# Kernel optimization log

Hardware: AMD Instinct MI355X
Metric: run time of the kernel (lower is better)

The kernel has to match this reference:

```python
import jax, jax.numpy as jnp
import numpy as np
import math

# ---- static circuit structure ----
N_QUBITS = 12
N_STATES = 1 << N_QUBITS
NUM_HEADS = 4
HEAD_DIM = N_QUBITS // NUM_HEADS
EPS = 1e-5

# convention: wire 0 = most significant bit of the basis index
_idx = np.arange(N_STATES)
_bits = (_idx[:, None] >> (N_QUBITS - 1 - np.arange(N_QUBITS))) & 1  # (N_STATES, n)
SIGNS = jnp.asarray((1 - 2 * _bits).astype(np.float32))  # +1 for |0>, -1 for |1>

# compose the CNOT ring [(0,1),(1,2),...,(n-2,n-1),(n-1,0)] into a single basis permutation.
# each CNOT(c,t) maps basis b -> b xor (bit_c(b) << pos_t); applying gate G: new[b] = old[sigma(b)].
_perm = _idx.copy()
_gates = [(i, i + 1) for i in range(N_QUBITS - 1)] + [(N_QUBITS - 1, 0)]
for _c, _t in reversed(_gates):
    _bc = (_idx >> (N_QUBITS - 1 - _c)) & 1
    _sigma = _idx ^ (_bc << (N_QUBITS - 1 - _t))
    _perm = _sigma[_perm]
PERM = jnp.asarray(_perm.astype(np.int32))
# second rx layer uses params token[wire % head_dim]
FOLD = np.arange(N_QUBITS) % HEAD_DIM


def _ring_z(theta):
    """Per-token circuit: RX(theta_k) on wire k (the two consecutive RX layers are
    pre-summed into theta), then CNOT ring, then <Z_k> for every wire.
    Product-state probabilities suffice: CNOTs only permute the computational basis.
    theta: (..., n_qubits) -> (..., n_qubits) expectation values."""
    shp = theta.shape
    T = theta.reshape(-1, N_QUBITS)
    h = 0.5 * T
    p0 = jnp.cos(h) ** 2  # P(|0>) per qubit after RX(theta)|0>
    p1 = jnp.sin(h) ** 2
    probs = jnp.ones((T.shape[0], 1), T.dtype)
    for k in range(N_QUBITS):  # kron build, wire 0 is MSB -> (tokens, 2^n)
        pk = jnp.stack([p0[:, k], p1[:, k]], axis=-1)
        probs = (probs[:, :, None] * pk[:, None, :]).reshape(T.shape[0], -1)
    probs = probs[:, PERM]  # apply CNOT ring as basis permutation
    return (probs @ SIGNS).reshape(shp)


def _layernorm(x, g, b):
    mu = jnp.mean(x, axis=-1, keepdims=True)
    var = jnp.mean((x - mu) ** 2, axis=-1, keepdims=True)
    return (x - mu) * jax.lax.rsqrt(var + EPS) * g + b


def _forward(x, wq, wk, wv, wo, w1, b1, w2, b2, g1, be1, g2, be2):
    B, S, E = x.shape
    # multi-head attention (dropout in eval mode = identity)
    q = (x @ wq).reshape(B, S, NUM_HEADS, HEAD_DIM).transpose(0, 2, 1, 3)
    k = (x @ wk).reshape(B, S, NUM_HEADS, HEAD_DIM).transpose(0, 2, 1, 3)
    v = (x @ wv).reshape(B, S, NUM_HEADS, HEAD_DIM).transpose(0, 2, 1, 3)
    scores = jnp.einsum('bhqd,bhkd->bhqk', q, k) / math.sqrt(HEAD_DIM)
    attn = jax.nn.softmax(scores, axis=-1)
    o = jnp.einsum('bhqk,bhkd->bhqd', attn, v).transpose(0, 2, 1, 3).reshape(B, S, E)
    # per-token quantum circuit: encoder RX(o_k) then RX(o_{k % head_dim}) combine additively
    theta = o + o[..., FOLD]
    attn_out = _ring_z(theta) @ wo
    x1 = _layernorm(x + attn_out, g1, be1)
    # quantum FFN: RX(h_k) then RY(h_k) on |0>, no entangler -> <Z_k> = cos(h_k)*cos(h_k)
    hdn = jax.nn.relu(x1 @ w1 + b1)
    zq = jnp.cos(hdn) * jnp.cos(hdn)
    ffn_out = zq @ w2 + b2
    return _layernorm(x1 + ffn_out, g2, be2)


def setup_inputs() -> dict:
    key = jax.random.key(0)
    ks = jax.random.split(key, 8)
    E = N_QUBITS
    F = N_QUBITS  # ffn_dim forced equal to n_qubits by the source
    s = 1.0 / math.sqrt(E)
    return {
        'x': jax.random.normal(ks[0], (4, 2048, E), jnp.float32),
        'wq': jax.random.normal(ks[1], (E, E), jnp.float32) * s,
        'wk': jax.random.normal(ks[2], (E, E), jnp.float32) * s,
        'wv': jax.random.normal(ks[3], (E, E), jnp.float32) * s,
        'wo': jax.random.normal(ks[4], (E, E), jnp.float32) * s,
        'w1': jax.random.normal(ks[5], (E, F), jnp.float32) * s,
        'b1': jnp.zeros((F,), jnp.float32),
        'w2': jax.random.normal(ks[6], (F, E), jnp.float32) * (1.0 / math.sqrt(F)),
        'b2': jnp.zeros((E,), jnp.float32),
        'g1': jnp.ones((E,), jnp.float32),
        'be1': jnp.zeros((E,), jnp.float32),
        'g2': jnp.ones((E,), jnp.float32),
        'be2': jnp.zeros((E,), jnp.float32),
    }


def reference(x, wq, wk, wv, wo, w1, b1, w2, b2, g1, be1, g2, be2):
    return _forward(x, wq, wk, wv, wo, w1, b1, w2, b2, g1, be1, g2, be2)
```

## Files before the change

### kernel.cpp

```cpp
#include <hip/hip_runtime.h>
#include <math.h>

#define S_LEN 2048
#define NH 4
#define BHN 16
#define E_DIM 12
#define NKB 8
#define KEYS_PER_KB (S_LEN / NKB)
#define NQT 8
#define QT_SIZE (S_LEN / NQT)
#define QSCALE 0.8329931278350429f

typedef float f32x2 __attribute__((ext_vector_type(2)));

static __device__ __forceinline__ f32x2 pk_mul_blo(f32x2 a, f32x2 b) {
    f32x2 d; asm("v_pk_mul_f32 %0, %1, %2 op_sel_hi:[1,0]"
                 : "=v"(d) : "v"(a), "v"(b)); return d;
}
static __device__ __forceinline__ f32x2 pk_fma_blo(f32x2 a, f32x2 b, f32x2 c) {
    f32x2 d; asm("v_pk_fma_f32 %0, %1, %2, %3 op_sel_hi:[1,0,1]"
                 : "=v"(d) : "v"(a), "v"(b), "v"(c)); return d;
}
static __device__ __forceinline__ f32x2 pk_fma_bhi(f32x2 a, f32x2 b, f32x2 c) {
    f32x2 d; asm("v_pk_fma_f32 %0, %1, %2, %3 op_sel:[0,1,0] op_sel_hi:[1,1,1]"
                 : "=v"(d) : "v"(a), "v"(b), "v"(c)); return d;
}
static __device__ __forceinline__ f32x2 pk_add2(f32x2 a, f32x2 b) {
    f32x2 d; asm("v_pk_add_f32 %0, %1, %2"
                 : "=v"(d) : "v"(a), "v"(b)); return d;
}

__global__ __launch_bounds__(256, 6) void attn_kernel(
    const float* __restrict__ x,
    const float* __restrict__ wq, const float* __restrict__ wk,
    const float* __restrict__ wv, float4* __restrict__ part)
{
    __shared__ __align__(16) char smem[16384];
    float4* sK  = (float4*)smem;
    float4* sV  = sK + KEYS_PER_KB;
    float4* sQ  = sV + KEYS_PER_KB;
    float*  sw  = (float*)(smem + 12288);
    float4* sAcc = (float4*)smem;

    int tid = threadIdx.x;
    int kb = blockIdx.x & (NKB - 1);
    int qt = (blockIdx.x / NKB) & (NQT - 1);
    int bh = blockIdx.x / (NKB * NQT);
    int b  = bh >> 2;
    int h  = bh & 3;

    if (tid < 108) {
        int m = tid / 36;
        int i = tid - m * 36;
        int e = i / 3, d = i - e * 3;
        const float* w = (m == 0) ? wq : (m == 1) ? wk : wv;
        sw[tid] = w[e * 12 + h * 3 + d];
    }
    __syncthreads();

    {
        size_t kt = (size_t)b * S_LEN + kb * KEYS_PER_KB + tid;
        const float4* xp = (const float4*)(x + kt * E_DIM);
        float4 xa = xp[0], xb = xp[1], xc = xp[2];
        float xr[12] = {xa.x, xa.y, xa.z, xa.w, xb.x, xb.y, xb.z, xb.w, xc.x, xc.y, xc.z, xc.w};
        float k0 = 0, k1 = 0, k2 = 0, v0 = 0, v1 = 0, v2 = 0;
#pragma unroll
        for (int e = 0; e < 12; ++e) {
            float xe = xr[e];
            k0 = fmaf(xe, sw[36 + e * 3 + 0], k0);
            k1 = fmaf(xe, sw[36 + e * 3 + 1], k1);
            k2 = fmaf(xe, sw[36 + e * 3 + 2], k2);
            v0 = fmaf(xe, sw[72 + e * 3 + 0], v0);
            v1 = fmaf(xe, sw[72 + e * 3 + 1], v1);
            v2 = fmaf(xe, sw[72 + e * 3 + 2], v2);
        }
        sK[tid] = make_float4(k0, k1, k2, 0.0f);
        sV[tid] = make_float4(v0, v1, v2, 0.0f);

        size_t qtk = (size_t)b * S_LEN + qt * QT_SIZE + tid;
        const float4* xq = (const float4*)(x + qtk * E_DIM);
        float4 qa = xq[0], qb = xq[1], qc = xq[2];
        float qr[12] = {qa.x, qa.y, qa.z, qa.w, qb.x, qb.y, qb.z, qb.w, qc.x, qc.y, qc.z, qc.w};
        float q0 = 0, q1 = 0, q2 = 0;
#pragma unroll
        for (int e = 0; e < 12; ++e) {
            float xe = qr[e];
            q0 = fmaf(xe, sw[e * 3 + 0], q0);
            q1 = fmaf(xe, sw[e * 3 + 1], q1);
            q2 = fmaf(xe, sw[e * 3 + 2], q2);
        }
        sQ[tid] = make_float4(q0 * QSCALE, q1 * QSCALE, q2 * QSCALE, 0.0f);
    }
    __syncthreads();

    int w = tid >> 6;
    int lane = tid & 63;

    float4 q0 = sQ[0 * 64 + lane];
    float4 q1 = sQ[1 * 64 + lane];
    float4 q2 = sQ[2 * 64 + lane];
    float4 q3 = sQ[3 * 64 + lane];
    f32x2 qx01 = {q0.x, q1.x}, qy01 = {q0.y, q1.y}, qz01 = {q0.z, q1.z};
    f32x2 qx23 = {q2.x, q3.x}, qy23 = {q2.y, q3.y}, qz23 = {q2.z, q3.z};

    f32x2 ax01 = {0,0}, ay01 = {0,0}, az01 = {0,0}, ad01 = {0,0};
    f32x2 ax23 = {0,0}, ay23 = {0,0}, az23 = {0,0}, ad23 = {0,0};

    int kbeg = w * 64;
#pragma unroll 4
    for (int j = 0; j < 64; ++j) {
        float4 kk = sK[kbeg + j];
        float4 vv = sV[kbeg + j];
        f32x2 kxy = {kk.x, kk.y};
        f32x2 kzw = {kk.z, kk.w};
        f32x2 vxy = {vv.x, vv.y};
        f32x2 vzw = {vv.z, vv.w};
        f32x2 s01 = pk_mul_blo(qz01, kzw);
        s01 = pk_fma_bhi(qy01, kxy, s01);
        s01 = pk_fma_blo(qx01, kxy, s01);
        f32x2 s23 = pk_mul_blo(qz23, kzw);
        s23 = pk_fma_bhi(qy23, kxy, s23);
        s23 = pk_fma_blo(qx23, kxy, s23);
        f32x2 p01, p23;
        p01.x = __builtin_amdgcn_exp2f(s01.x);
        p01.y = __builtin_amdgcn_exp2f(s01.y);
        p23.x = __builtin_amdgcn_exp2f(s23.x);
        p23.y = __builtin_amdgcn_exp2f(s23.y);
        ax01 = pk_fma_blo(p01, vxy, ax01);
        ay01 = pk_fma_bhi(p01, vxy, ay01);
        az01 = pk_fma_blo(p01, vzw, az01);
        ad01 = pk_add2(p01, ad01);
        ax23 = pk_fma_blo(p23, vxy, ax23);
        ay23 = pk_fma_bhi(p23, vxy, ay23);
        az23 = pk_fma_blo(p23, vzw, az23);
        ad23 = pk_add2(p23, ad23);
    }

    __syncthreads();
    sAcc[w * QT_SIZE + 0 * 64 + lane] = make_float4(ax01.x, ay01.x, az01.x, ad01.x);
    sAcc[w * QT_SIZE + 1 * 64 + lane] = make_float4(ax01.y, ay01.y, az01.y, ad01.y);
    sAcc[w * QT_SIZE + 2 * 64 + lane] = make_float4(ax23.x, ay23.x, az23.x, ad23.x);
    sAcc[w * QT_SIZE + 3 * 64 + lane] = make_float4(ax23.y, ay23.y, az23.y, ad23.y);
    __syncthreads();

    float4 sum = sAcc[tid];
    float4 p1 = sAcc[QT_SIZE + tid];
    float4 p2 = sAcc[2 * QT_SIZE + tid];
    float4 p3 = sAcc[3 * QT_SIZE + tid];
    sum.x += p1.x + p2.x + p3.x;
    sum.y += p1.y + p2.y + p3.y;
    sum.z += p1.z + p2.z + p3.z;
    sum.w += p1.w + p2.w + p3.w;

    part[((size_t)kb * BHN + bh) * S_LEN + qt * QT_SIZE + tid] = sum;
}

__global__ __launch_bounds__(64) void tail_kernel(
    const float4* __restrict__ part, const float* __restrict__ x,
    const float* __restrict__ wo, const float* __restrict__ w1, const float* __restrict__ b1,
    const float* __restrict__ w2, const float* __restrict__ b2,
    const float* __restrict__ g1, const float* __restrict__ be1,
    const float* __restrict__ g2, const float* __restrict__ be2,
    float* __restrict__ out)
{
    __shared__ float swo[144], sw1[144], sw2[144];
    __shared__ float sb1[12], sb2[12], sg1[12], sbe1[12], sg2[12], sbe2[12];
    int tid = threadIdx.x;
    for (int i = tid; i < 144; i += 64) { swo[i] = wo[i]; sw1[i] = w1[i]; sw2[i] = w2[i]; }
    if (tid < 12) {
        sb1[tid] = b1[tid]; sb2[tid] = b2[tid];
        sg1[tid] = g1[tid]; sbe1[tid] = be1[tid];
        sg2[tid] = g2[tid]; sbe2[tid] = be2[tid];
    }
    __syncthreads();

    int t = blockIdx.x * 64 + tid;
    int b = t >> 11;
    int s = t & (S_LEN - 1);

    float o[12];
#pragma unroll
    for (int h = 0; h < NH; ++h) {
        int bh = b * NH + h;
        float ax = 0, ay = 0, az = 0, aw = 0;
#pragma unroll
        for (int kb = 0; kb < NKB; ++kb) {
            float4 p = part[((size_t)kb * BHN + bh) * S_LEN + s];
            ax += p.x; ay += p.y; az += p.z; aw += p.w;
        }
        float inv = 1.0f / aw;
        o[h * 3 + 0] = ax * inv;
        o[h * 3 + 1] = ay * inv;
        o[h * 3 + 2] = az * inv;
    }

    float c[12];
#pragma unroll
    for (int k = 0; k < 12; ++k) c[k] = __cosf(o[k] + o[k % 3]);

    float z[12];
    {
        float p = c[0];
#pragma unroll
        for (int k = 1; k < 12; ++k) { p *= c[k]; z[k] = p; }
        p = c[1];
#pragma unroll
        for (int k = 2; k < 12; ++k) p *= c[k];
        z[0] = p;
    }

    const float4* xp = (const float4*)(x + (size_t)t * E_DIM);
    float4 xa = xp[0], xb = xp[1], xc = xp[2];
    float xr[12] = {xa.x, xa.y, xa.z, xa.w, xb.x, xb.y, xb.z, xb.w, xc.x, xc.y, xc.z, xc.w};

    float y[12];
#pragma unroll
    for (int e = 0; e < 12; ++e) {
        float ao = 0;
#pragma unroll
        for (int k = 0; k < 12; ++k) ao = fmaf(z[k], swo[k * 12 + e], ao);
        y[e] = xr[e] + ao;
    }

    float mu = 0;
#pragma unroll
    for (int e = 0; e < 12; ++e) mu += y[e];
    mu *= (1.0f / 12.0f);
    float var = 0;
#pragma unroll
    for (int e = 0; e < 12; ++e) { float d = y[e] - mu; var = fmaf(d, d, var); }
    var *= (1.0f / 12.0f);
    float rs = rsqrtf(var + 1e-5f);
    float x1v[12];
#pragma unroll
    for (int e = 0; e < 12; ++e) x1v[e] = (y[e] - mu) * rs * sg1[e] + sbe1[e];

    float zq[12];
#pragma unroll
    for (int f = 0; f < 12; ++f) {
        float hd = sb1[f];
#pragma unroll
        for (int e = 0; e < 12; ++e) hd = fmaf(x1v[e], sw1[e * 12 + f], hd);
        hd = fmaxf(hd, 0.0f);
        float cc = __cosf(hd);
        zq[f] = cc * cc;
    }
    float y2[12];
#pragma unroll
    for (int e = 0; e < 12; ++e) {
        float fo = sb2[e];
#pragma unroll
        for (int f = 0; f < 12; ++f) fo = fmaf(zq[f], sw2[f * 12 + e], fo);
        y2[e] = x1v[e] + fo;
    }

    float mu2 = 0;
#pragma unroll
    for (int e = 0; e < 12; ++e) mu2 += y2[e];
    mu2 *= (1.0f / 12.0f);
    float var2 = 0;
#pragma unroll
    for (int e = 0; e < 12; ++e) { float d = y2[e] - mu2; var2 = fmaf(d, d, var2); }
    var2 *= (1.0f / 12.0f);
    float rs2 = rsqrtf(var2 + 1e-5f);

    float res[12];
#pragma unroll
    for (int e = 0; e < 12; ++e) res[e] = (y2[e] - mu2) * rs2 * sg2[e] + sbe2[e];

    float4* op = (float4*)(out + (size_t)t * E_DIM);
    op[0] = make_float4(res[0], res[1], res[2], res[3]);
    op[1] = make_float4(res[4], res[5], res[6], res[7]);
    op[2] = make_float4(res[8], res[9], res[10], res[11]);
}

extern "C" void kernel_launch(void* const* d_in, const int* in_sizes, int n_in,
                              void* d_out, int out_size, void* d_ws, size_t ws_size,
                              hipStream_t stream)
{
    const float* x   = (const float*)d_in[0];
    const float* wq  = (const float*)d_in[1];
    const float* wk  = (const float*)d_in[2];
    const float* wv  = (const float*)d_in[3];
    const float* wo  = (const float*)d_in[4];
    const float* w1  = (const float*)d_in[5];
    const float* b1  = (const float*)d_in[6];
    const float* w2  = (const float*)d_in[7];
    const float* b2  = (const float*)d_in[8];
    const float* g1  = (const float*)d_in[9];
    const float* be1 = (const float*)d_in[10];
    const float* g2  = (const float*)d_in[11];
    const float* be2 = (const float*)d_in[12];

    float4* part = (float4*)d_ws;

    attn_kernel<<<BHN * NQT * NKB, 256, 0, stream>>>(x, wq, wk, wv, part);
    tail_kernel<<<128, 64, 0, stream>>>(part, x, wo, w1, b1, w2, b2,
                                        g1, be1, g2, be2, (float*)d_out);
}
```

Before: 25.91 us.

## Fuse tail into attention kernel via last-block atomic counter, halve query tiles

Merges the separate tail kernel into the attention kernel. Each block writes its partial with non-temporal stores and bumps an atomic counter per (batch, query tile); the 32nd block to finish reduces the partials and runs the output projection, layernorms and FFN. The query tile is doubled to 512 (NQT 4), so each thread handles 8 queries per key and the grid shrinks to 512 blocks. This removes one kernel launch and overlaps the tail with attention, but adds a memset launch, serialises the tail on a few last blocks, and raises register pressure.

```diff
diff --git a/kernel.cpp b/kernel.cpp
--- a/kernel.cpp
+++ b/kernel.cpp
@@ -7,11 +7,12 @@
 #define E_DIM 12
 #define NKB 8
 #define KEYS_PER_KB (S_LEN / NKB)
-#define NQT 8
+#define NQT 4
 #define QT_SIZE (S_LEN / NQT)
 #define QSCALE 0.8329931278350429f
 
 typedef float f32x2 __attribute__((ext_vector_type(2)));
+typedef float f32x4 __attribute__((ext_vector_type(4)));
 
 static __device__ __forceinline__ f32x2 pk_mul_blo(f32x2 a, f32x2 b) {
     f32x2 d; asm("v_pk_mul_f32 %0, %1, %2 op_sel_hi:[1,0]"
@@ -30,17 +31,50 @@
                  : "=v"(d) : "v"(a), "v"(b)); return d;
 }
 
-__global__ __launch_bounds__(256, 6) void attn_kernel(
+static __device__ __forceinline__ void store_nt(f32x4* p, f32x4 v) {
+    asm volatile("global_store_dwordx4 %0, %1, off sc0 sc1 nt"
+                 :: "v"(p), "v"(v) : "memory");
+}
+static __device__ __forceinline__ f32x4 load_sc_issue(const f32x4* p) {
+    f32x4 d;
+    asm volatile("global_load_dwordx4 %0, %1, off sc0 sc1"
+                 : "=v"(d) : "v"(p) : "memory");
+    return d;
+}
+
+#define PAIR_STEP(QX,QY,QZ,AX,AY,AZ,AD) do {                       \
+    f32x2 s_ = pk_mul_blo(QZ, kzw);                                \
+    s_ = pk_fma_bhi(QY, kxy, s_);                                  \
+    s_ = pk_fma_blo(QX, kxy, s_);                                  \
+    f32x2 p_;                                                      \
+    p_.x = __builtin_amdgcn_exp2f(s_.x);                           \
+    p_.y = __builtin_amdgcn_exp2f(s_.y);                           \
+    AX = pk_fma_blo(p_, vxy, AX);                                  \
+    AY = pk_fma_bhi(p_, vxy, AY);                                  \
+    AZ = pk_fma_blo(p_, vzw, AZ);                                  \
+    AD = pk_add2(p_, AD);                                          \
+} while (0)
+
+__global__ __launch_bounds__(256) void attn_fused_kernel(
     const float* __restrict__ x,
     const float* __restrict__ wq, const float* __restrict__ wk,
-    const float* __restrict__ wv, float4* __restrict__ part)
+    const float* __restrict__ wv, const float* __restrict__ wo,
+    const float* __restrict__ w1, const float* __restrict__ b1,
+    const float* __restrict__ w2, const float* __restrict__ b2,
+    const float* __restrict__ g1, const float* __restrict__ be1,
+    const float* __restrict__ g2, const float* __restrict__ be2,
+    f32x4* __restrict__ part, unsigned int* __restrict__ counter,
+    float* __restrict__ out)
 {
-    __shared__ __align__(16) char smem[16384];
-    float4* sK  = (float4*)smem;
-    float4* sV  = sK + KEYS_PER_KB;
-    float4* sQ  = sV + KEYS_PER_KB;
-    float*  sw  = (float*)(smem + 12288);
+    __shared__ __align__(16) char smem[32768];
+    float4* sK = (float4*)smem;
+    float4* sV = sK + KEYS_PER_KB;
+    float4* sQ = sV + KEYS_PER_KB;
+    float*  sw = (float*)(smem + 16384);
     float4* sAcc = (float4*)smem;
+    __shared__ float swo[144], sw1[144], sw2[144];
+    __shared__ float sb1[12], sb2[12], sg1[12], sbe1[12], sg2[12], sbe2[12];
+    __shared__ int sLast;
 
     int tid = threadIdx.x;
     int kb = blockIdx.x & (NKB - 1);
@@ -77,96 +111,94 @@
         sK[tid] = make_float4(k0, k1, k2, 0.0f);
         sV[tid] = make_float4(v0, v1, v2, 0.0f);
 
-        size_t qtk = (size_t)b * S_LEN + qt * QT_SIZE + tid;
-        const float4* xq = (const float4*)(x + qtk * E_DIM);
-        float4 qa = xq[0], qb = xq[1], qc = xq[2];
-        float qr[12] = {qa.x, qa.y, qa.z, qa.w, qb.x, qb.y, qb.z, qb.w, qc.x, qc.y, qc.z, qc.w};
-        float q0 = 0, q1 = 0, q2 = 0;
-#pragma unroll
-        for (int e = 0; e < 12; ++e) {
-            float xe = qr[e];
-            q0 = fmaf(xe, sw[e * 3 + 0], q0);
-            q1 = fmaf(xe, sw[e * 3 + 1], q1);
-            q2 = fmaf(xe, sw[e * 3 + 2], q2);
-        }
-        sQ[tid] = make_float4(q0 * QSCALE, q1 * QSCALE, q2 * QSCALE, 0.0f);
+#pragma unroll
+        for (int rr = 0; rr < 2; ++rr) {
+            int qi = rr * 256 + tid;
+            size_t qtk = (size_t)b * S_LEN + qt * QT_SIZE + qi;
+            const float4* xq = (const float4*)(x + qtk * E_DIM);
+            float4 qa = xq[0], qb = xq[1], qc = xq[2];
+            float qr[12] = {qa.x, qa.y, qa.z, qa.w, qb.x, qb.y, qb.z, qb.w, qc.x, qc.y, qc.z, qc.w};
+            float q0 = 0, q1 = 0, q2 = 0;
+#pragma unroll
+            for (int e = 0; e < 12; ++e) {
+                float xe = qr[e];
+                q0 = fmaf(xe, sw[e * 3 + 0], q0);
+                q1 = fmaf(xe, sw[e * 3 + 1], q1);
+                q2 = fmaf(xe, sw[e * 3 + 2], q2);
+            }
+            sQ[qi] = make_float4(q0 * QSCALE, q1 * QSCALE, q2 * QSCALE, 0.0f);
+        }
     }
     __syncthreads();
 
     int w = tid >> 6;
     int lane = tid & 63;
 
-    float4 q0 = sQ[0 * 64 + lane];
-    float4 q1 = sQ[1 * 64 + lane];
-    float4 q2 = sQ[2 * 64 + lane];
-    float4 q3 = sQ[3 * 64 + lane];
+    float4 q0 = sQ[0 * 64 + lane], q1 = sQ[1 * 64 + lane];
+    float4 q2 = sQ[2 * 64 + lane], q3 = sQ[3 * 64 + lane];
+    float4 q4 = sQ[4 * 64 + lane], q5 = sQ[5 * 64 + lane];
+    float4 q6 = sQ[6 * 64 + lane], q7 = sQ[7 * 64 + lane];
     f32x2 qx01 = {q0.x, q1.x}, qy01 = {q0.y, q1.y}, qz01 = {q0.z, q1.z};
     f32x2 qx23 = {q2.x, q3.x}, qy23 = {q2.y, q3.y}, qz23 = {q2.z, q3.z};
+    f32x2 qx45 = {q4.x, q5.x}, qy45 = {q4.y, q5.y}, qz45 = {q4.z, q5.z};
+    f32x2 qx67 = {q6.x, q7.x}, qy67 = {q6.y, q7.y}, qz67 = {q6.z, q7.z};
 
     f32x2 ax01 = {0,0}, ay01 = {0,0}, az01 = {0,0}, ad01 = {0,0};
     f32x2 ax23 = {0,0}, ay23 = {0,0}, az23 = {0,0}, ad23 = {0,0};
+    f32x2 ax45 = {0,0}, ay45 = {0,0}, az45 = {0,0}, ad45 = {0,0};
+    f32x2 ax67 = {0,0}, ay67 = {0,0}, az67 = {0,0}, ad67 = {0,0};
 
     int kbeg = w * 64;
-#pragma unroll 4
+#pragma unroll 2
     for (int j = 0; j < 64; ++j) {
         float4 kk = sK[kbeg + j];
         float4 vv = sV[kbeg + j];
-        f32x2 kxy = {kk.x, kk.y};
-        f32x2 kzw = {kk.z, kk.w};
-        f32x2 vxy = {vv.x, vv.y};
-        f32x2 vzw = {vv.z, vv.w};
-        f32x2 s01 = pk_mul_blo(qz01, kzw);
-        s01 = pk_fma_bhi(qy01, kxy, s01);
-        s01 = pk_fma_blo(qx01, kxy, s01);
-        f32x2 s23 = pk_mul_blo(qz23, kzw);
-        s23 = pk_fma_bhi(qy23, kxy, s23);
-        s23 = pk_fma_blo(qx23, kxy, s23);
-        f32x2 p01, p23;
-        p01.x = __builtin_amdgcn_exp2f(s01.x);
-        p01.y = __builtin_amdgcn_exp2f(s01.y);
-        p23.x = __builtin_amdgcn_exp2f(s23.x);
-        p23.y = __builtin_amdgcn_exp2f(s23.y);
-        ax01 = pk_fma_blo(p01, vxy, ax01);
-        ay01 = pk_fma_bhi(p01, vxy, ay01);
-        az01 = pk_fma_blo(p01, vzw, az01);
-        ad01 = pk_add2(p01, ad01);
-        ax23 = pk_fma_blo(p23, vxy, ax23);
-        ay23 = pk_fma_bhi(p23, vxy, ay23);
-        az23 = pk_fma_blo(p23, vzw, az23);
-        ad23 = pk_add2(p23, ad23);
-    }
-
-    __syncthreads();
-    sAcc[w * QT_SIZE + 0 * 64 + lane] = make_float4(ax01.x, ay01.x, az01.x, ad01.x);
-    sAcc[w * QT_SIZE + 1 * 64 + lane] = make_float4(ax01.y, ay01.y, az01.y, ad01.y);
-    sAcc[w * QT_SIZE + 2 * 64 + lane] = make_float4(ax23.x, ay23.x, az23.x, ad23.x);
-    sAcc[w * QT_SIZE + 3 * 64 + lane] = make_float4(ax23.y, ay23.y, az23.y, ad23.y);
-    __syncthreads();
-
-    float4 sum = sAcc[tid];
-    float4 p1 = sAcc[QT_SIZE + tid];
-    float4 p2 = sAcc[2 * QT_SIZE + tid];
-    float4 p3 = sAcc[3 * QT_SIZE + tid];
-    sum.x += p1.x + p2.x + p3.x;
-    sum.y += p1.y + p2.y + p3.y;
-    sum.z += p1.z + p2.z + p3.z;
-    sum.w += p1.w + p2.w + p3.w;
-
-    part[((size_t)kb * BHN + bh) * S_LEN + qt * QT_SIZE + tid] = sum;
-}
-
-__global__ __launch_bounds__(64) void tail_kernel(
-    const float4* __restrict__ part, const float* __restrict__ x,
-    const float* __restrict__ wo, const float* __restrict__ w1, const float* __restrict__ b1,
-    const float* __restrict__ w2, const float* __restrict__ b2,
-    const float* __restrict__ g1, const float* __restrict__ be1,
-    const float* __restrict__ g2, const float* __restrict__ be2,
-    float* __restrict__ out)
-{
-    __shared__ float swo[144], sw1[144], sw2[144];
-    __shared__ float sb1[12], sb2[12], sg1[12], sbe1[12], sg2[12], sbe2[12];
-    int tid = threadIdx.x;
-    for (int i = tid; i < 144; i += 64) { swo[i] = wo[i]; sw1[i] = w1[i]; sw2[i] = w2[i]; }
+        f32x2 kxy = {kk.x, kk.y}, kzw = {kk.z, kk.w};
+        f32x2 vxy = {vv.x, vv.y}, vzw = {vv.z, vv.w};
+        PAIR_STEP(qx01, qy01, qz01, ax01, ay01, az01, ad01);
+        PAIR_STEP(qx23, qy23, qz23, ax23, ay23, az23, ad23);
+        PAIR_STEP(qx45, qy45, qz45, ax45, ay45, az45, ad45);
+        PAIR_STEP(qx67, qy67, qz67, ax67, ay67, az67, ad67);
+    }
+
+    __syncthreads();
+    {
+        float4* a = sAcc + w * QT_SIZE + lane;
+        a[0 * 64] = make_float4(ax01.x, ay01.x, az01.x, ad01.x);
+        a[1 * 64] = make_float4(ax01.y, ay01.y, az01.y, ad01.y);
+        a[2 * 64] = make_float4(ax23.x, ay23.x, az23.x, ad23.x);
+        a[3 * 64] = make_float4(ax23.y, ay23.y, az23.y, ad23.y);
+        a[4 * 64] = make_float4(ax45.x, ay45.x, az45.x, ad45.x);
+        a[5 * 64] = make_float4(ax45.y, ay45.y, az45.y, ad45.y);
+        a[6 * 64] = make_float4(ax67.x, ay67.x, az67.x, ad67.x);
+        a[7 * 64] = make_float4(ax67.y, ay67.y, az67.y, ad67.y);
+    }
+    __syncthreads();
+
+#pragma unroll
+    for (int rr = 0; rr < 2; ++rr) {
+        int qq = rr * 256 + tid;
+        float4 sum = sAcc[qq];
+        float4 p1 = sAcc[QT_SIZE + qq];
+        float4 p2 = sAcc[2 * QT_SIZE + qq];
+        float4 p3 = sAcc[3 * QT_SIZE + qq];
+        f32x4 sv;
+        sv.x = sum.x + (p1.x + p2.x + p3.x);
+        sv.y = sum.y + (p1.y + p2.y + p3.y);
+        sv.z = sum.z + (p1.z + p2.z + p3.z);
+        sv.w = sum.w + (p1.w + p2.w + p3.w);
+        store_nt(part + ((size_t)kb * BHN + bh) * S_LEN + qt * QT_SIZE + qq, sv);
+    }
+    __syncthreads();
+
+    if (tid == 0) {
+        unsigned old = atomicAdd(&counter[b * NQT + qt], 1u);
+        sLast = (old == 31u);
+    }
+    __syncthreads();
+    if (!sLast) return;
+
+    for (int i = tid; i < 144; i += 256) { swo[i] = wo[i]; sw1[i] = w1[i]; sw2[i] = w2[i]; }
     if (tid < 12) {
         sb1[tid] = b1[tid]; sb2[tid] = b2[tid];
         sg1[tid] = g1[tid]; sbe1[tid] = be1[tid];
@@ -174,104 +206,119 @@
     }
     __syncthreads();
 
-    int t = blockIdx.x * 64 + tid;
-    int b = t >> 11;
-    int s = t & (S_LEN - 1);
-
-    float o[12];
-#pragma unroll
-    for (int h = 0; h < NH; ++h) {
-        int bh = b * NH + h;
-        float ax = 0, ay = 0, az = 0, aw = 0;
-#pragma unroll
-        for (int kb = 0; kb < NKB; ++kb) {
-            float4 p = part[((size_t)kb * BHN + bh) * S_LEN + s];
-            ax += p.x; ay += p.y; az += p.z; aw += p.w;
-        }
-        float inv = 1.0f / aw;
-        o[h * 3 + 0] = ax * inv;
-        o[h * 3 + 1] = ay * inv;
-        o[h * 3 + 2] = az * inv;
-    }
-
-    float c[12];
-#pragma unroll
-    for (int k = 0; k < 12; ++k) c[k] = __cosf(o[k] + o[k % 3]);
-
-    float z[12];
-    {
-        float p = c[0];
-#pragma unroll
-        for (int k = 1; k < 12; ++k) { p *= c[k]; z[k] = p; }
-        p = c[1];
-#pragma unroll
-        for (int k = 2; k < 12; ++k) p *= c[k];
-        z[0] = p;
-    }
-
-    const float4* xp = (const float4*)(x + (size_t)t * E_DIM);
-    float4 xa = xp[0], xb = xp[1], xc = xp[2];
-    float xr[12] = {xa.x, xa.y, xa.z, xa.w, xb.x, xb.y, xb.z, xb.w, xc.x, xc.y, xc.z, xc.w};
-
-    float y[12];
-#pragma unroll
-    for (int e = 0; e < 12; ++e) {
-        float ao = 0;
-#pragma unroll
-        for (int k = 0; k < 12; ++k) ao = fmaf(z[k], swo[k * 12 + e], ao);
-        y[e] = xr[e] + ao;
-    }
-
-    float mu = 0;
-#pragma unroll
-    for (int e = 0; e < 12; ++e) mu += y[e];
-    mu *= (1.0f / 12.0f);
-    float var = 0;
-#pragma unroll
-    for (int e = 0; e < 12; ++e) { float d = y[e] - mu; var = fmaf(d, d, var); }
-    var *= (1.0f / 12.0f);
-    float rs = rsqrtf(var + 1e-5f);
-    float x1v[12];
-#pragma unroll
-    for (int e = 0; e < 12; ++e) x1v[e] = (y[e] - mu) * rs * sg1[e] + sbe1[e];
-
-    float zq[12];
-#pragma unroll
-    for (int f = 0; f < 12; ++f) {
-        float hd = sb1[f];
-#pragma unroll
-        for (int e = 0; e < 12; ++e) hd = fmaf(x1v[e], sw1[e * 12 + f], hd);
-        hd = fmaxf(hd, 0.0f);
-        float cc = __cosf(hd);
-        zq[f] = cc * cc;
-    }
-    float y2[12];
-#pragma unroll
-    for (int e = 0; e < 12; ++e) {
-        float fo = sb2[e];
-#pragma unroll
-        for (int f = 0; f < 12; ++f) fo = fmaf(zq[f], sw2[f * 12 + e], fo);
-        y2[e] = x1v[e] + fo;
-    }
-
-    float mu2 = 0;
-#pragma unroll
-    for (int e = 0; e < 12; ++e) mu2 += y2[e];
-    mu2 *= (1.0f / 12.0f);
-    float var2 = 0;
-#pragma unroll
-    for (int e = 0; e < 12; ++e) { float d = y2[e] - mu2; var2 = fmaf(d, d, var2); }
-    var2 *= (1.0f / 12.0f);
-    float rs2 = rsqrtf(var2 + 1e-5f);
-
-    float res[12];
-#pragma unroll
-    for (int e = 0; e < 12; ++e) res[e] = (y2[e] - mu2) * rs2 * sg2[e] + sbe2[e];
-
-    float4* op = (float4*)(out + (size_t)t * E_DIM);
-    op[0] = make_float4(res[0], res[1], res[2], res[3]);
-    op[1] = make_float4(res[4], res[5], res[6], res[7]);
-    op[2] = make_float4(res[8], res[9], res[10], res[11]);
+    int bb4 = b * NH;
+#pragma unroll
+    for (int rr = 0; rr < 2; ++rr) {
+        int idx = rr * 256 + tid;
+        int ss  = qt * QT_SIZE + idx;
+        int t   = b * S_LEN + ss;
+
+        float o[12];
+#pragma unroll
+        for (int hp = 0; hp < 2; ++hp) {
+            f32x4 L[16];
+#pragma unroll
+            for (int i = 0; i < 16; ++i) {
+                int kb2 = i & 7, hh = hp * 2 + (i >> 3);
+                L[i] = load_sc_issue(part + ((size_t)kb2 * BHN + bb4 + hh) * S_LEN + ss);
+            }
+            asm volatile("s_waitcnt vmcnt(0)" ::: "memory");
+            __builtin_amdgcn_sched_barrier(0);
+#pragma unroll
+            for (int hh2 = 0; hh2 < 2; ++hh2) {
+                float ax = 0, ay = 0, az = 0, aw = 0;
+#pragma unroll
+                for (int i2 = 0; i2 < 8; ++i2) {
+                    f32x4 p = L[hh2 * 8 + i2];
+                    ax += p.x; ay += p.y; az += p.z; aw += p.w;
+                }
+                float inv = 1.0f / aw;
+                int h3 = (hp * 2 + hh2) * 3;
+                o[h3 + 0] = ax * inv;
+                o[h3 + 1] = ay * inv;
+                o[h3 + 2] = az * inv;
+            }
+        }
+
+        float c[12];
+#pragma unroll
+        for (int k = 0; k < 12; ++k) c[k] = __cosf(o[k] + o[k % 3]);
+
+        float z[12];
+        {
+            float p = c[0];
+#pragma unroll
+            for (int k = 1; k < 12; ++k) { p *= c[k]; z[k] = p; }
+            p = c[1];
+#pragma unroll
+            for (int k = 2; k < 12; ++k) p *= c[k];
+            z[0] = p;
+        }
+
+        const float4* xp = (const float4*)(x + (size_t)t * E_DIM);
+        float4 xa = xp[0], xb = xp[1], xc = xp[2];
+        float xr[12] = {xa.x, xa.y, xa.z, xa.w, xb.x, xb.y, xb.z, xb.w, xc.x, xc.y, xc.z, xc.w};
+
+        float y[12];
+#pragma unroll
+        for (int e = 0; e < 12; ++e) {
+            float ao = 0;
+#pragma unroll
+            for (int k = 0; k < 12; ++k) ao = fmaf(z[k], swo[k * 12 + e], ao);
+            y[e] = xr[e] + ao;
+        }
+
+        float mu = 0;
+#pragma unroll
+        for (int e = 0; e < 12; ++e) mu += y[e];
+        mu *= (1.0f / 12.0f);
+        float var = 0;
+#pragma unroll
+        for (int e = 0; e < 12; ++e) { float d = y[e] - mu; var = fmaf(d, d, var); }
+        var *= (1.0f / 12.0f);
+        float rs = rsqrtf(var + 1e-5f);
+        float x1v[12];
+#pragma unroll
+        for (int e = 0; e < 12; ++e) x1v[e] = (y[e] - mu) * rs * sg1[e] + sbe1[e];
+
+        float zq[12];
+#pragma unroll
+        for (int f = 0; f < 12; ++f) {
+            float hd = sb1[f];
+#pragma unroll
+            for (int e = 0; e < 12; ++e) hd = fmaf(x1v[e], sw1[e * 12 + f], hd);
+            hd = fmaxf(hd, 0.0f);
+            float cc = __cosf(hd);
+            zq[f] = cc * cc;
+        }
+        float y2[12];
+#pragma unroll
+        for (int e = 0; e < 12; ++e) {
+            float fo = sb2[e];
+#pragma unroll
+            for (int f = 0; f < 12; ++f) fo = fmaf(zq[f], sw2[f * 12 + e], fo);
+            y2[e] = x1v[e] + fo;
+        }
+
+        float mu2 = 0;
+#pragma unroll
+        for (int e = 0; e < 12; ++e) mu2 += y2[e];
+        mu2 *= (1.0f / 12.0f);
+        float var2 = 0;
+#pragma unroll
+        for (int e = 0; e < 12; ++e) { float d = y2[e] - mu2; var2 = fmaf(d, d, var2); }
+        var2 *= (1.0f / 12.0f);
+        float rs2 = rsqrtf(var2 + 1e-5f);
+
+        float res[12];
+#pragma unroll
+        for (int e = 0; e < 12; ++e) res[e] = (y2[e] - mu2) * rs2 * sg2[e] + sbe2[e];
+
+        float4* op = (float4*)(out + (size_t)t * E_DIM);
+        op[0] = make_float4(res[0], res[1], res[2], res[3]);
+        op[1] = make_float4(res[4], res[5], res[6], res[7]);
+        op[2] = make_float4(res[8], res[9], res[10], res[11]);
+    }
 }
 
 extern "C" void kernel_launch(void* const* d_in, const int* in_sizes, int n_in,
@@ -292,9 +339,11 @@
     const float* g2  = (const float*)d_in[11];
     const float* be2 = (const float*)d_in[12];
 
-    float4* part = (float4*)d_ws;
-
-    attn_kernel<<<BHN * NQT * NKB, 256, 0, stream>>>(x, wq, wk, wv, part);
-    tail_kernel<<<128, 64, 0, stream>>>(part, x, wo, w1, b1, w2, b2,
-                                        g1, be1, g2, be2, (float*)d_out);
-}
+    f32x4* part = (f32x4*)d_ws;
+    unsigned int* counter = (unsigned int*)((char*)d_ws + (size_t)NKB * BHN * S_LEN * 16);
+
+    (void)hipMemsetAsync(counter, 0, 16 * sizeof(unsigned int), stream);
+    attn_fused_kernel<<<BHN * NQT * NKB, 256, 0, stream>>>(
+        x, wq, wk, wv, wo, w1, b1, w2, b2, g1, be1, g2, be2,
+        part, counter, (float*)d_out);
+}
```

After: 40.00 us. 54.4% more time.
